# Optimization experiments

Hardware: AMD Instinct MI355X
Metric: run time of the kernel (lower is better)

## Reference

```python
import jax, jax.numpy as jnp
import numpy as np

D_MODEL = 1024
NUM_HEADS = 16
D_K = D_MODEL // NUM_HEADS
D_FF = 4096
EPS = 1e-5


def _layernorm(x, gamma, beta):
    mu = jnp.mean(x, axis=-1, keepdims=True)
    var = jnp.mean(jnp.square(x - mu), axis=-1, keepdims=True)
    return (x - mu) * jax.lax.rsqrt(var + EPS) * gamma + beta


def setup_inputs() -> dict:
    key = jax.random.key(0)
    ks = jax.random.split(key, 16)
    B, S = 4, 2048
    s_in = 1.0 / np.sqrt(D_MODEL)
    s_ff = 1.0 / np.sqrt(D_FF)
    inp = {
        "x": jax.random.normal(ks[0], (B, S, D_MODEL), jnp.float32),
        "src_mask": jnp.ones((B, 1, 1, S), jnp.int32),
        "w_q": jax.random.normal(ks[1], (D_MODEL, D_MODEL), jnp.float32) * s_in,
        "b_q": jnp.zeros((D_MODEL,), jnp.float32),
        "w_k": jax.random.normal(ks[2], (D_MODEL, D_MODEL), jnp.float32) * s_in,
        "b_k": jnp.zeros((D_MODEL,), jnp.float32),
        "w_v": jax.random.normal(ks[3], (D_MODEL, D_MODEL), jnp.float32) * s_in,
        "b_v": jnp.zeros((D_MODEL,), jnp.float32),
        "w_o": jax.random.normal(ks[4], (D_MODEL, D_MODEL), jnp.float32) * s_in,
        "b_o": jnp.zeros((D_MODEL,), jnp.float32),
        "w1": jax.random.normal(ks[5], (D_MODEL, D_FF), jnp.float32) * s_in,
        "b1": jnp.zeros((D_FF,), jnp.float32),
        "w2": jax.random.normal(ks[6], (D_FF, D_MODEL), jnp.float32) * s_ff,
        "b2": jnp.zeros((D_MODEL,), jnp.float32),
        "g1": jnp.ones((D_MODEL,), jnp.float32),
        "be1": jnp.zeros((D_MODEL,), jnp.float32),
        "g2": jnp.ones((D_MODEL,), jnp.float32),
        "be2": jnp.zeros((D_MODEL,), jnp.float32),
    }
    return inp


def reference(x, src_mask, w_q, b_q, w_k, b_k, w_v, b_v, w_o, b_o,
              w1, b1, w2, b2, g1, be1, g2, be2):
    B, S, _ = x.shape

    def split_heads(t):  # [B,S,D] -> [B,H,S,dk]
        return t.reshape(B, S, NUM_HEADS, D_K).transpose(0, 2, 1, 3)

    q = split_heads(x @ w_q + b_q)
    k = split_heads(x @ w_k + b_k)
    v = split_heads(x @ w_v + b_v)

    scores = jnp.einsum("bhqd,bhkd->bhqk", q, k) / np.sqrt(D_K)
    scores = jnp.where(src_mask == 0, -jnp.inf, scores)
    attn = jax.nn.softmax(scores, axis=-1)
    ctx = jnp.einsum("bhqk,bhkd->bhqd", attn, v)
    merged = ctx.transpose(0, 2, 1, 3).reshape(B, S, D_MODEL)
    attn_out = merged @ w_o + b_o

    h = _layernorm(x + attn_out, g1, be1)
    ff = jax.nn.relu(h @ w1 + b1) @ w2 + b2
    return _layernorm(h + ff, g2, be2)
```

## Files before the change

### kernel.cpp

```cpp
#include <hip/hip_runtime.h>

typedef unsigned short u16;
typedef __attribute__((ext_vector_type(4))) unsigned short u16x4;
typedef __attribute__((ext_vector_type(8))) short bf16x8;
typedef __attribute__((ext_vector_type(4))) float f32x4;

__device__ inline float bf2f(u16 u) {
  union { unsigned int i; float f; } v; v.i = ((unsigned int)u) << 16; return v.f;
}
__device__ inline u16 f2bf(float f) {
  union { float f; unsigned int i; } v; v.f = f;
  unsigned int r = v.i + 0x7fffu + ((v.i >> 16) & 1u);
  return (u16)(r >> 16);
}
__device__ inline unsigned int cvt_pk_bf16(float lo, float hi) {
  unsigned int r;
  asm("v_cvt_pk_bf16_f32 %0, %1, %2" : "=v"(r) : "v"(lo), "v"(hi));
  return r;
}

typedef const __attribute__((address_space(1))) unsigned int* gas_t;
typedef __attribute__((address_space(3))) unsigned int* las_t;
__device__ inline void gload_lds16(const u16* g, u16* l) {
  __builtin_amdgcn_global_load_lds((gas_t)(unsigned long long)(const void*)g,
                                   (las_t)(unsigned int)(unsigned long long)(void*)l,
                                   16, 0, 0);
}

__global__ __launch_bounds__(256) void cvt_bf16(const float* __restrict__ src,
                                                u16* __restrict__ dst, int n) {
  int i = (blockIdx.x * 256 + threadIdx.x) * 4;
  if (i >= n) return;
  float4 v = *(const float4*)(src + i);
  u16x4 o;
  o.x = f2bf(v.x); o.y = f2bf(v.y); o.z = f2bf(v.z); o.w = f2bf(v.w);
  *(u16x4*)(dst + i) = o;
}

__global__ __launch_bounds__(256) void concat3(const float* __restrict__ a,
                                               const float* __restrict__ b,
                                               const float* __restrict__ c,
                                               float* __restrict__ o, int n) {
  int i = blockIdx.x * 256 + threadIdx.x;
  if (i >= n) return;
  o[i] = a[i]; o[n + i] = b[i]; o[2 * n + i] = c[i];
}

__global__ __launch_bounds__(256) void transpose_f32_bf16(const float* __restrict__ src,
                                                          u16* __restrict__ dst,
                                                          int R, int C) {
  __shared__ u16 tile[32][33];
  int tx = threadIdx.x & 31, ty = threadIdx.x >> 5;
  int c0 = blockIdx.x * 32, r0 = blockIdx.y * 32;
  #pragma unroll
  for (int i = ty; i < 32; i += 8)
    tile[i][tx] = f2bf(src[(size_t)(r0 + i) * C + c0 + tx]);
  __syncthreads();
  #pragma unroll
  for (int i = ty; i < 32; i += 8)
    dst[(size_t)(c0 + i) * R + r0 + tx] = tile[tx][i];
}

__global__ __launch_bounds__(256) void transpose_v(const u16* __restrict__ src,
                                                   u16* __restrict__ VT,
                                                   int B, int S, int H, int RS, int CO) {
  __shared__ u16 tile[32][33];
  int tx = threadIdx.x & 31, ty = threadIdx.x >> 5;
  int s0 = blockIdx.x * 32, d0 = blockIdx.y * 32;
  int bh = blockIdx.z;
  int b = bh / H, h = bh % H;
  #pragma unroll
  for (int i = ty; i < 32; i += 8)
    tile[i][tx] = src[(size_t)(b * S + s0 + i) * RS + CO + h * 64 + d0 + tx];
  __syncthreads();
  #pragma unroll
  for (int i = ty; i < 32; i += 8)
    VT[((size_t)bh * 64 + d0 + i) * S + s0 + tx] = tile[tx][i];
}

__global__ __launch_bounds__(256) void gemm_bt(const u16* __restrict__ A,
                                               const u16* __restrict__ Bt,
                                               const float* __restrict__ bias,
                                               u16* __restrict__ C,
                                               int M, int N, int K, int relu) {
  __shared__ u16 As[128 * 32];
  __shared__ u16 Bs[128 * 32];
  const int tid = threadIdx.x;
  const int lane = tid & 63, wid = tid >> 6;
  const int lr = lane & 15, quad = lane >> 4;
  const int wm = (wid >> 1) * 64, wn = (wid & 1) * 64;
  const int m0 = blockIdx.y * 128, n0 = blockIdx.x * 128;
  const int lrow = lane >> 2;
  const int lcol = (lane & 3) * 8;

  f32x4 acc[4][4];
  const f32x4 zero = {0.f, 0.f, 0.f, 0.f};
  #pragma unroll
  for (int mt = 0; mt < 4; ++mt)
    #pragma unroll
    for (int nt = 0; nt < 4; ++nt) acc[mt][nt] = zero;

  for (int k0 = 0; k0 < K; k0 += 32) {
    #pragma unroll
    for (int it = 0; it < 2; ++it) {
      int rbase = wid * 32 + it * 16;
      gload_lds16(A + (size_t)(m0 + rbase + lrow) * K + k0 + lcol, &As[rbase * 32]);
      gload_lds16(Bt + (size_t)(n0 + rbase + lrow) * K + k0 + lcol, &Bs[rbase * 32]);
    }
    __syncthreads();
    bf16x8 af[4], bfr[4];
    #pragma unroll
    for (int mt = 0; mt < 4; ++mt)
      af[mt] = *(const bf16x8*)(&As[(wm + mt * 16 + lr) * 32 + quad * 8]);
    #pragma unroll
    for (int nt = 0; nt < 4; ++nt)
      bfr[nt] = *(const bf16x8*)(&Bs[(wn + nt * 16 + lr) * 32 + quad * 8]);
    #pragma unroll
    for (int mt = 0; mt < 4; ++mt)
      #pragma unroll
      for (int nt = 0; nt < 4; ++nt)
        acc[mt][nt] = __builtin_amdgcn_mfma_f32_16x16x32_bf16(af[mt], bfr[nt], acc[mt][nt], 0, 0, 0);
    __syncthreads();
  }

  #pragma unroll
  for (int nt = 0; nt < 4; ++nt) {
    int n = n0 + wn + nt * 16 + lr;
    float bv = bias[n];
    #pragma unroll
    for (int mt = 0; mt < 4; ++mt) {
      #pragma unroll
      for (int i = 0; i < 4; ++i) {
        int m = m0 + wm + mt * 16 + quad * 4 + i;
        float v = acc[mt][nt][i] + bv;
        if (relu) v = fmaxf(v, 0.f);
        C[(size_t)m * N + n] = f2bf(v);
      }
    }
  }
}

__global__ __launch_bounds__(256) void flash_attn(const u16* __restrict__ Qp,
                                                  const u16* __restrict__ Kp,
                                                  const u16* __restrict__ VT,
                                                  const int* __restrict__ mask,
                                                  u16* __restrict__ ctx,
                                                  int B, int S, int H, int QSTR) {
  __shared__ u16 kt_lds[64 * 64];
  __shared__ u16 vt_lds[64 * 64];
  __shared__ u16 p_lds[4 * 16 * 72];
  __shared__ float msk_lds[64];
  const int tid = threadIdx.x;
  const int lane = tid & 63, wid = tid >> 6;
  const int lr = lane & 15, quad = lane >> 4;
  const int bh = blockIdx.y;
  const int b = bh / H, h = bh % H;
  const int q0 = blockIdx.x * 64;
  const u16* vt_base = VT + (size_t)bh * 64 * S;
  const float SC = 0.125f * 1.44269504089f;

  const int srl = lane >> 3;
  const int scol = ((lane & 7) ^ srl) * 8;
  const int swz = (lr & 7) << 3;

  bf16x8 qf[2];
  {
    int qm = q0 + wid * 16 + lr;
    const u16* qptr = Qp + (size_t)(b * S + qm) * QSTR + h * 64;
    qf[0] = *(const bf16x8*)(qptr + quad * 8);
    qf[1] = *(const bf16x8*)(qptr + 32 + quad * 8);
  }

  float m_i = -1e30f, l_i = 0.f;
  f32x4 O[4];
  #pragma unroll
  for (int nt = 0; nt < 4; ++nt) {
    O[nt][0] = 0.f; O[nt][1] = 0.f; O[nt][2] = 0.f; O[nt][3] = 0.f;
  }

  u16* pw = &p_lds[wid * 16 * 72];
  const u16* kgp = Kp + ((size_t)b * S + wid * 16 + srl) * QSTR + h * 64 + scol;
  const u16* vgp = vt_base + (size_t)(wid * 16 + srl) * S + scol;
  u16* klb = &kt_lds[(wid * 16) * 64];
  u16* vlb = &vt_lds[(wid * 16) * 64];

  for (int kt = 0; kt < S; kt += 64) {
    gload_lds16(kgp + (size_t)kt * QSTR, klb);
    gload_lds16(kgp + (size_t)(kt + 8) * QSTR, klb + 8 * 64);
    gload_lds16(vgp + kt, vlb);
    gload_lds16(vgp + 8 * (size_t)S + kt, vlb + 8 * 64);
    if (tid < 64) msk_lds[tid] = mask[b * S + kt + tid] ? 0.f : -1e30f;
    __syncthreads();

    float s[4][4];
    __builtin_amdgcn_s_setprio(1);
    #pragma unroll
    for (int st = 0; st < 4; ++st) {
      f32x4 c = {0.f, 0.f, 0.f, 0.f};
      const u16* kr = &kt_lds[(st * 16 + lr) * 64];
      bf16x8 kf0 = *(const bf16x8*)(kr + ((quad * 8) ^ swz));
      bf16x8 kf1 = *(const bf16x8*)(kr + ((32 + quad * 8) ^ swz));
      c = __builtin_amdgcn_mfma_f32_16x16x32_bf16(kf0, qf[0], c, 0, 0, 0);
      c = __builtin_amdgcn_mfma_f32_16x16x32_bf16(kf1, qf[1], c, 0, 0, 0);
      float4 mv = *(const float4*)(&msk_lds[st * 16 + quad * 4]);
      s[st][0] = c[0] * SC + mv.x;
      s[st][1] = c[1] * SC + mv.y;
      s[st][2] = c[2] * SC + mv.z;
      s[st][3] = c[3] * SC + mv.w;
    }
    __builtin_amdgcn_s_setprio(0);

    float tmax = s[0][0];
    #pragma unroll
    for (int st = 0; st < 4; ++st)
      #pragma unroll
      for (int i = 0; i < 4; ++i) tmax = fmaxf(tmax, s[st][i]);
    tmax = fmaxf(tmax, __shfl_xor(tmax, 16, 64));
    tmax = fmaxf(tmax, __shfl_xor(tmax, 32, 64));
    if (__any(tmax > m_i + 8.0f)) {
      float mn = fmaxf(m_i, tmax);
      float al = exp2f(m_i - mn);
      m_i = mn;
      l_i *= al;
      #pragma unroll
      for (int nt = 0; nt < 4; ++nt) {
        O[nt][0] *= al; O[nt][1] *= al; O[nt][2] *= al; O[nt][3] *= al;
      }
    }
    float rs = 0.f;
    #pragma unroll
    for (int st = 0; st < 4; ++st)
      #pragma unroll
      for (int i = 0; i < 4; ++i) {
        float p = exp2f(s[st][i] - m_i);
        s[st][i] = p; rs += p;
      }
    l_i += rs;

    #pragma unroll
    for (int st = 0; st < 4; ++st) {
      uint2 pk;
      pk.x = cvt_pk_bf16(s[st][0], s[st][1]);
      pk.y = cvt_pk_bf16(s[st][2], s[st][3]);
      *(uint2*)(&pw[lr * 72 + st * 16 + quad * 4]) = pk;
    }

    bf16x8 pf0 = *(const bf16x8*)(&pw[lr * 72 + quad * 8]);
    bf16x8 pf1 = *(const bf16x8*)(&pw[lr * 72 + 32 + quad * 8]);
    __builtin_amdgcn_s_setprio(1);
    #pragma unroll
    for (int nt = 0; nt < 4; ++nt) {
      const u16* vr = &vt_lds[(nt * 16 + lr) * 64];
      bf16x8 vf0 = *(const bf16x8*)(vr + ((quad * 8) ^ swz));
      bf16x8 vf1 = *(const bf16x8*)(vr + ((32 + quad * 8) ^ swz));
      O[nt] = __builtin_amdgcn_mfma_f32_16x16x32_bf16(vf0, pf0, O[nt], 0, 0, 0);
      O[nt] = __builtin_amdgcn_mfma_f32_16x16x32_bf16(vf1, pf1, O[nt], 0, 0, 0);
    }
    __builtin_amdgcn_s_setprio(0);
    __syncthreads();
  }

  l_i += __shfl_xor(l_i, 16, 64);
  l_i += __shfl_xor(l_i, 32, 64);
  float linv = 1.f / fmaxf(l_i, 1e-30f);
  int q = q0 + wid * 16 + lr;
  u16* op = ctx + (size_t)(b * S + q) * (H * 64) + h * 64;
  #pragma unroll
  for (int nt = 0; nt < 4; ++nt) {
    u16x4 o;
    o.x = f2bf(O[nt][0] * linv); o.y = f2bf(O[nt][1] * linv);
    o.z = f2bf(O[nt][2] * linv); o.w = f2bf(O[nt][3] * linv);
    *(u16x4*)(op + nt * 16 + quad * 4) = o;
  }
}

__device__ inline float block_reduce_sum(float v, float* sbuf) {
  #pragma unroll
  for (int m = 1; m < 64; m <<= 1) v += __shfl_xor(v, m, 64);
  int w = threadIdx.x >> 6;
  if ((threadIdx.x & 63) == 0) sbuf[w] = v;
  __syncthreads();
  v = sbuf[0] + sbuf[1] + sbuf[2] + sbuf[3];
  __syncthreads();
  return v;
}

__global__ __launch_bounds__(256) void add_ln(const float* __restrict__ a32,
                                              const u16* __restrict__ a16,
                                              const u16* __restrict__ b,
                                              const float* __restrict__ g,
                                              const float* __restrict__ be,
                                              u16* __restrict__ out16,
                                              float* __restrict__ out32, int D) {
  __shared__ float sbuf[4];
  int row = blockIdx.x;
  size_t base = (size_t)row * D;
  int i = threadIdx.x * 4;
  float v[4];
  {
    u16x4 bv = *(const u16x4*)(b + base + i);
    if (a32) {
      float4 av = *(const float4*)(a32 + base + i);
      v[0] = av.x + bf2f(bv.x); v[1] = av.y + bf2f(bv.y);
      v[2] = av.z + bf2f(bv.z); v[3] = av.w + bf2f(bv.w);
    } else {
      u16x4 av = *(const u16x4*)(a16 + base + i);
      v[0] = bf2f(av.x) + bf2f(bv.x); v[1] = bf2f(av.y) + bf2f(bv.y);
      v[2] = bf2f(av.z) + bf2f(bv.z); v[3] = bf2f(av.w) + bf2f(bv.w);
    }
  }
  float sum = v[0] + v[1] + v[2] + v[3];
  sum = block_reduce_sum(sum, sbuf);
  float mean = sum / (float)D;
  float var = 0.f;
  #pragma unroll
  for (int j = 0; j < 4; ++j) { float d = v[j] - mean; var += d * d; }
  var = block_reduce_sum(var, sbuf);
  float rstd = rsqrtf(var / (float)D + 1e-5f);
  float4 gv = *(const float4*)(g + i);
  float4 bev = *(const float4*)(be + i);
  float o0 = (v[0] - mean) * rstd * gv.x + bev.x;
  float o1 = (v[1] - mean) * rstd * gv.y + bev.y;
  float o2 = (v[2] - mean) * rstd * gv.z + bev.z;
  float o3 = (v[3] - mean) * rstd * gv.w + bev.w;
  if (out32) {
    float4 o = {o0, o1, o2, o3};
    *(float4*)(out32 + base + i) = o;
  } else {
    u16x4 o;
    o.x = f2bf(o0); o.y = f2bf(o1); o.z = f2bf(o2); o.w = f2bf(o3);
    *(u16x4*)(out16 + base + i) = o;
  }
}

extern "C" void kernel_launch(void* const* d_in, const int* in_sizes, int n_in,
                              void* d_out, int out_size, void* d_ws, size_t ws_size,
                              hipStream_t stream) {
  (void)in_sizes; (void)n_in; (void)out_size; (void)ws_size;
  const float* x   = (const float*)d_in[0];
  const int* mask  = (const int*)d_in[1];
  const float* wq  = (const float*)d_in[2];
  const float* bq  = (const float*)d_in[3];
  const float* wk  = (const float*)d_in[4];
  const float* bk  = (const float*)d_in[5];
  const float* wv  = (const float*)d_in[6];
  const float* bv  = (const float*)d_in[7];
  const float* wo  = (const float*)d_in[8];
  const float* bo  = (const float*)d_in[9];
  const float* w1  = (const float*)d_in[10];
  const float* b1  = (const float*)d_in[11];
  const float* w2  = (const float*)d_in[12];
  const float* b2  = (const float*)d_in[13];
  const float* g1  = (const float*)d_in[14];
  const float* be1 = (const float*)d_in[15];
  const float* g2  = (const float*)d_in[16];
  const float* be2 = (const float*)d_in[17];

  const int B = 4, S = 2048, D = 1024, H = 16, DFF = 4096;
  const int D3 = 3 * D;
  const size_t TOK = (size_t)B * S;
  const size_t TD = TOK * D;

  u16* ws   = (u16*)d_ws;
  u16* QKVp = ws;
  u16* xb   = ws + 3 * TD;
  u16* VT   = xb;
  u16* CTX  = ws + 4 * TD;
  u16* ATT  = ws + 5 * TD;
  u16* Hb   = ws + 6 * TD;
  u16* QKVT = ws + 7 * TD;
  u16* WOT  = QKVT + 3 * (size_t)D * D;
  u16* W1T  = WOT + (size_t)D * D;
  u16* FF1  = ws;
  u16* FF2  = ATT;
  u16* W2T  = QKVT;
  float* biasc = (float*)CTX;

  dim3 blk(256);

  cvt_bf16<<<dim3((unsigned)(TD / (256 * 4))), blk, 0, stream>>>(x, xb, (int)TD);
  concat3<<<dim3(4), blk, 0, stream>>>(bq, bk, bv, biasc, D);

  transpose_f32_bf16<<<dim3(D / 32, D / 32), blk, 0, stream>>>(wq, QKVT, D, D);
  transpose_f32_bf16<<<dim3(D / 32, D / 32), blk, 0, stream>>>(wk, QKVT + (size_t)D * D, D, D);
  transpose_f32_bf16<<<dim3(D / 32, D / 32), blk, 0, stream>>>(wv, QKVT + 2 * (size_t)D * D, D, D);
  transpose_f32_bf16<<<dim3(D / 32, D / 32), blk, 0, stream>>>(wo, WOT, D, D);
  transpose_f32_bf16<<<dim3(DFF / 32, D / 32), blk, 0, stream>>>(w1, W1T, D, DFF);

  gemm_bt<<<dim3(D3 / 128, TOK / 128), blk, 0, stream>>>(xb, QKVT, biasc, QKVp, (int)TOK, D3, D, 0);

  transpose_v<<<dim3(S / 32, 2, B * H), blk, 0, stream>>>(QKVp, VT, B, S, H, D3, 2 * D);

  flash_attn<<<dim3(S / 64, B * H), blk, 0, stream>>>(QKVp, QKVp + D, VT, mask, CTX, B, S, H, D3);

  gemm_bt<<<dim3(D / 128, TOK / 128), blk, 0, stream>>>(CTX, WOT, bo, ATT, (int)TOK, D, D, 0);

  transpose_f32_bf16<<<dim3(D / 32, DFF / 32), blk, 0, stream>>>(w2, W2T, DFF, D);

  add_ln<<<dim3((unsigned)TOK), blk, 0, stream>>>(x, (const u16*)nullptr, ATT, g1, be1,
                                                  Hb, (float*)nullptr, D);

  gemm_bt<<<dim3(DFF / 128, TOK / 128), blk, 0, stream>>>(Hb, W1T, b1, FF1, (int)TOK, DFF, D, 1);
  gemm_bt<<<dim3(D / 128, TOK / 128), blk, 0, stream>>>(FF1, W2T, b2, FF2, (int)TOK, D, DFF, 0);

  add_ln<<<dim3((unsigned)TOK), blk, 0, stream>>>((const float*)nullptr, Hb, FF2, g2, be2,
                                                  (u16*)nullptr, (float*)d_out, D);
}
```

Before: 659.0 us.

## Double-buffer K/V tiles in flash attention and prefetch mask into registers

The flash attention kernel now keeps two LDS buffers for the K and V tiles and issues the next tile's global-to-LDS loads before computing on the current one. This overlaps memory latency with the MFMA work and leaves one barrier per iteration instead of a load-then-sync pattern. The mask is prefetched directly into registers instead of being staged through LDS. The P scratch buffer switches from padded rows to an XOR swizzle, which shrinks its LDS footprint. LDS use still roughly doubles for K/V, which may reduce occupancy. The prefetch also relies on the single trailing barrier being enough to guard buffer reuse, and it is not obvious the async loads are complete before the next iteration reads them.

```diff
diff --git a/kernel.cpp b/kernel.cpp
--- a/kernel.cpp
+++ b/kernel.cpp
@@ -146,10 +146,9 @@
                                                   const int* __restrict__ mask,
                                                   u16* __restrict__ ctx,
                                                   int B, int S, int H, int QSTR) {
-  __shared__ u16 kt_lds[64 * 64];
-  __shared__ u16 vt_lds[64 * 64];
-  __shared__ u16 p_lds[4 * 16 * 72];
-  __shared__ float msk_lds[64];
+  __shared__ u16 kt_lds[2][64 * 64];
+  __shared__ u16 vt_lds[2][64 * 64];
+  __shared__ u16 p_lds[4 * 16 * 64];
   const int tid = threadIdx.x;
   const int lane = tid & 63, wid = tid >> 6;
   const int lr = lane & 15, quad = lane >> 4;
@@ -157,6 +156,7 @@
   const int b = bh / H, h = bh % H;
   const int q0 = blockIdx.x * 64;
   const u16* vt_base = VT + (size_t)bh * 64 * S;
+  const int* mbase = mask + b * S;
   const float SC = 0.125f * 1.44269504089f;
 
   const int srl = lane >> 3;
@@ -178,35 +178,57 @@
     O[nt][0] = 0.f; O[nt][1] = 0.f; O[nt][2] = 0.f; O[nt][3] = 0.f;
   }
 
-  u16* pw = &p_lds[wid * 16 * 72];
+  u16* pw = &p_lds[wid * 16 * 64 + lr * 64];
   const u16* kgp = Kp + ((size_t)b * S + wid * 16 + srl) * QSTR + h * 64 + scol;
   const u16* vgp = vt_base + (size_t)(wid * 16 + srl) * S + scol;
-  u16* klb = &kt_lds[(wid * 16) * 64];
-  u16* vlb = &vt_lds[(wid * 16) * 64];
-
+  u16* klb0 = &kt_lds[0][(wid * 16) * 64];
+  u16* vlb0 = &vt_lds[0][(wid * 16) * 64];
+  u16* klb1 = &kt_lds[1][(wid * 16) * 64];
+  u16* vlb1 = &vt_lds[1][(wid * 16) * 64];
+
+  gload_lds16(kgp, klb0);
+  gload_lds16(kgp + 8 * (size_t)QSTR, klb0 + 8 * 64);
+  gload_lds16(vgp, vlb0);
+  gload_lds16(vgp + 8 * (size_t)S, vlb0 + 8 * 64);
+  int4 mk_nxt[4];
+  #pragma unroll
+  for (int st = 0; st < 4; ++st)
+    mk_nxt[st] = *(const int4*)(mbase + st * 16 + quad * 4);
+  __syncthreads();
+
+  int cur = 0;
   for (int kt = 0; kt < S; kt += 64) {
-    gload_lds16(kgp + (size_t)kt * QSTR, klb);
-    gload_lds16(kgp + (size_t)(kt + 8) * QSTR, klb + 8 * 64);
-    gload_lds16(vgp + kt, vlb);
-    gload_lds16(vgp + 8 * (size_t)S + kt, vlb + 8 * 64);
-    if (tid < 64) msk_lds[tid] = mask[b * S + kt + tid] ? 0.f : -1e30f;
-    __syncthreads();
+    int4 mk[4];
+    #pragma unroll
+    for (int st = 0; st < 4; ++st) mk[st] = mk_nxt[st];
+    if (kt + 64 < S) {
+      u16* klb = cur ? klb0 : klb1;
+      u16* vlb = cur ? vlb0 : vlb1;
+      gload_lds16(kgp + (size_t)(kt + 64) * QSTR, klb);
+      gload_lds16(kgp + (size_t)(kt + 72) * QSTR, klb + 8 * 64);
+      gload_lds16(vgp + kt + 64, vlb);
+      gload_lds16(vgp + 8 * (size_t)S + kt + 64, vlb + 8 * 64);
+      #pragma unroll
+      for (int st = 0; st < 4; ++st)
+        mk_nxt[st] = *(const int4*)(mbase + kt + 64 + st * 16 + quad * 4);
+    }
+    const u16* kl = kt_lds[cur];
+    const u16* vl = vt_lds[cur];
 
     float s[4][4];
     __builtin_amdgcn_s_setprio(1);
     #pragma unroll
     for (int st = 0; st < 4; ++st) {
       f32x4 c = {0.f, 0.f, 0.f, 0.f};
-      const u16* kr = &kt_lds[(st * 16 + lr) * 64];
+      const u16* kr = &kl[(st * 16 + lr) * 64];
       bf16x8 kf0 = *(const bf16x8*)(kr + ((quad * 8) ^ swz));
       bf16x8 kf1 = *(const bf16x8*)(kr + ((32 + quad * 8) ^ swz));
       c = __builtin_amdgcn_mfma_f32_16x16x32_bf16(kf0, qf[0], c, 0, 0, 0);
       c = __builtin_amdgcn_mfma_f32_16x16x32_bf16(kf1, qf[1], c, 0, 0, 0);
-      float4 mv = *(const float4*)(&msk_lds[st * 16 + quad * 4]);
-      s[st][0] = c[0] * SC + mv.x;
-      s[st][1] = c[1] * SC + mv.y;
-      s[st][2] = c[2] * SC + mv.z;
-      s[st][3] = c[3] * SC + mv.w;
+      s[st][0] = c[0] * SC + (mk[st].x ? 0.f : -1e30f);
+      s[st][1] = c[1] * SC + (mk[st].y ? 0.f : -1e30f);
+      s[st][2] = c[2] * SC + (mk[st].z ? 0.f : -1e30f);
+      s[st][3] = c[3] * SC + (mk[st].w ? 0.f : -1e30f);
     }
     __builtin_amdgcn_s_setprio(0);
 
@@ -242,22 +264,24 @@
       uint2 pk;
       pk.x = cvt_pk_bf16(s[st][0], s[st][1]);
       pk.y = cvt_pk_bf16(s[st][2], s[st][3]);
-      *(uint2*)(&pw[lr * 72 + st * 16 + quad * 4]) = pk;
-    }
-
-    bf16x8 pf0 = *(const bf16x8*)(&pw[lr * 72 + quad * 8]);
-    bf16x8 pf1 = *(const bf16x8*)(&pw[lr * 72 + 32 + quad * 8]);
+      *(uint2*)(&pw[(st * 16 + quad * 4) ^ swz]) = pk;
+    }
+
+    bf16x8 pf0 = *(const bf16x8*)(&pw[(quad * 8) ^ swz]);
+    bf16x8 pf1 = *(const bf16x8*)(&pw[(32 + quad * 8) ^ swz]);
     __builtin_amdgcn_s_setprio(1);
     #pragma unroll
     for (int nt = 0; nt < 4; ++nt) {
-      const u16* vr = &vt_lds[(nt * 16 + lr) * 64];
+      const u16* vr = &vl[(nt * 16 + lr) * 64];
       bf16x8 vf0 = *(const bf16x8*)(vr + ((quad * 8) ^ swz));
       bf16x8 vf1 = *(const bf16x8*)(vr + ((32 + quad * 8) ^ swz));
       O[nt] = __builtin_amdgcn_mfma_f32_16x16x32_bf16(vf0, pf0, O[nt], 0, 0, 0);
       O[nt] = __builtin_amdgcn_mfma_f32_16x16x32_bf16(vf1, pf1, O[nt], 0, 0, 0);
     }
     __builtin_amdgcn_s_setprio(0);
+
     __syncthreads();
+    cur ^= 1;
   }
 
   l_i += __shfl_xor(l_i, 16, 64);
```

Measured after the change: 696.0 us. +5.6%, slower.

## Rewrite flash attention with 32x32x16 MFMA, register P, 128-query blocks

Applied to the files above, without the earlier changes.

The flash attention kernel moves from 16x16x32 to 32x32x16 MFMA tiles. Each wave now owns 32 queries, so a block covers 128 queries and each K/V tile loaded into LDS is reused across twice as many queries. The probability matrix is repacked between lanes with cross-half shuffles instead of a round trip through LDS. The mask is now a ballot that is applied only when some key is masked, and the rescale threshold now works on unscaled scores. This cuts LDS traffic, global K/V loads and the grid size, at the cost of more registers and fewer blocks, which may lower occupancy.

```diff
diff --git a/kernel.cpp b/kernel.cpp
--- a/kernel.cpp
+++ b/kernel.cpp
@@ -4,6 +4,7 @@
 typedef __attribute__((ext_vector_type(4))) unsigned short u16x4;
 typedef __attribute__((ext_vector_type(8))) short bf16x8;
 typedef __attribute__((ext_vector_type(4))) float f32x4;
+typedef __attribute__((ext_vector_type(16))) float f32x16;
 
 __device__ inline float bf2f(u16 u) {
   union { unsigned int i; float f; } v; v.i = ((unsigned int)u) << 16; return v.f;
@@ -17,6 +18,12 @@
   unsigned int r;
   asm("v_cvt_pk_bf16_f32 %0, %1, %2" : "=v"(r) : "v"(lo), "v"(hi));
   return r;
+}
+__device__ inline f32x16 zero16() {
+  f32x16 z;
+  #pragma unroll
+  for (int i = 0; i < 16; ++i) z[i] = 0.f;
+  return z;
 }
 
 typedef const __attribute__((address_space(1))) unsigned int* gas_t;
@@ -148,37 +155,31 @@
                                                   int B, int S, int H, int QSTR) {
   __shared__ u16 kt_lds[64 * 64];
   __shared__ u16 vt_lds[64 * 64];
-  __shared__ u16 p_lds[4 * 16 * 72];
-  __shared__ float msk_lds[64];
   const int tid = threadIdx.x;
   const int lane = tid & 63, wid = tid >> 6;
-  const int lr = lane & 15, quad = lane >> 4;
+  const int l31 = lane & 31, hi = lane >> 5;
   const int bh = blockIdx.y;
   const int b = bh / H, h = bh % H;
-  const int q0 = blockIdx.x * 64;
   const u16* vt_base = VT + (size_t)bh * 64 * S;
+  const int* mbase = mask + b * S;
   const float SC = 0.125f * 1.44269504089f;
 
   const int srl = lane >> 3;
   const int scol = ((lane & 7) ^ srl) * 8;
-  const int swz = (lr & 7) << 3;
-
-  bf16x8 qf[2];
+  const int rsw = (lane & 7) << 3;
+
+  const int q = blockIdx.x * 128 + wid * 32 + l31;
+  bf16x8 qf[4];
   {
-    int qm = q0 + wid * 16 + lr;
-    const u16* qptr = Qp + (size_t)(b * S + qm) * QSTR + h * 64;
-    qf[0] = *(const bf16x8*)(qptr + quad * 8);
-    qf[1] = *(const bf16x8*)(qptr + 32 + quad * 8);
+    const u16* qptr = Qp + (size_t)(b * S + q) * QSTR + h * 64;
+    #pragma unroll
+    for (int t = 0; t < 4; ++t)
+      qf[t] = *(const bf16x8*)(qptr + t * 16 + hi * 8);
   }
 
   float m_i = -1e30f, l_i = 0.f;
-  f32x4 O[4];
-  #pragma unroll
-  for (int nt = 0; nt < 4; ++nt) {
-    O[nt][0] = 0.f; O[nt][1] = 0.f; O[nt][2] = 0.f; O[nt][3] = 0.f;
-  }
-
-  u16* pw = &p_lds[wid * 16 * 72];
+  f32x16 o0 = zero16(), o1 = zero16();
+
   const u16* kgp = Kp + ((size_t)b * S + wid * 16 + srl) * QSTR + h * 64 + scol;
   const u16* vgp = vt_base + (size_t)(wid * 16 + srl) * S + scol;
   u16* klb = &kt_lds[(wid * 16) * 64];
@@ -189,88 +190,108 @@
     gload_lds16(kgp + (size_t)(kt + 8) * QSTR, klb + 8 * 64);
     gload_lds16(vgp + kt, vlb);
     gload_lds16(vgp + 8 * (size_t)S + kt, vlb + 8 * 64);
-    if (tid < 64) msk_lds[tid] = mask[b * S + kt + tid] ? 0.f : -1e30f;
+    int mv = mbase[kt + lane];
+    unsigned long long bal = __ballot(mv != 0);
     __syncthreads();
 
-    float s[4][4];
+    f32x16 sa0 = zero16(), sa1 = zero16();
+    const u16* krow0 = &kt_lds[l31 * 64];
+    const u16* krow1 = &kt_lds[(32 + l31) * 64];
     __builtin_amdgcn_s_setprio(1);
     #pragma unroll
-    for (int st = 0; st < 4; ++st) {
-      f32x4 c = {0.f, 0.f, 0.f, 0.f};
-      const u16* kr = &kt_lds[(st * 16 + lr) * 64];
-      bf16x8 kf0 = *(const bf16x8*)(kr + ((quad * 8) ^ swz));
-      bf16x8 kf1 = *(const bf16x8*)(kr + ((32 + quad * 8) ^ swz));
-      c = __builtin_amdgcn_mfma_f32_16x16x32_bf16(kf0, qf[0], c, 0, 0, 0);
-      c = __builtin_amdgcn_mfma_f32_16x16x32_bf16(kf1, qf[1], c, 0, 0, 0);
-      float4 mv = *(const float4*)(&msk_lds[st * 16 + quad * 4]);
-      s[st][0] = c[0] * SC + mv.x;
-      s[st][1] = c[1] * SC + mv.y;
-      s[st][2] = c[2] * SC + mv.z;
-      s[st][3] = c[3] * SC + mv.w;
+    for (int dblock = 0; dblock < 4; ++dblock) {
+      int c = (dblock * 16 + hi * 8) ^ rsw;
+      bf16x8 kf0 = *(const bf16x8*)(krow0 + c);
+      bf16x8 kf1 = *(const bf16x8*)(krow1 + c);
+      sa0 = __builtin_amdgcn_mfma_f32_32x32x16_bf16(kf0, qf[dblock], sa0, 0, 0, 0);
+      sa1 = __builtin_amdgcn_mfma_f32_32x32x16_bf16(kf1, qf[dblock], sa1, 0, 0, 0);
     }
     __builtin_amdgcn_s_setprio(0);
 
-    float tmax = s[0][0];
-    #pragma unroll
-    for (int st = 0; st < 4; ++st)
+    if (bal != 0xFFFFFFFFFFFFFFFFull) {
+      unsigned long long balh = bal >> (hi * 4);
       #pragma unroll
-      for (int i = 0; i < 4; ++i) tmax = fmaxf(tmax, s[st][i]);
-    tmax = fmaxf(tmax, __shfl_xor(tmax, 16, 64));
+      for (int r = 0; r < 16; ++r) {
+        int kloc = (r & 3) + 8 * (r >> 2);
+        if (!((balh >> kloc) & 1)) sa0[r] = -2e30f;
+        if (!((balh >> (32 + kloc)) & 1)) sa1[r] = -2e30f;
+      }
+    }
+
+    float tmax = sa0[0];
+    #pragma unroll
+    for (int r = 1; r < 16; ++r) tmax = fmaxf(tmax, sa0[r]);
+    #pragma unroll
+    for (int r = 0; r < 16; ++r) tmax = fmaxf(tmax, sa1[r]);
     tmax = fmaxf(tmax, __shfl_xor(tmax, 32, 64));
-    if (__any(tmax > m_i + 8.0f)) {
+    if (__any(tmax > m_i + 44.0f)) {
       float mn = fmaxf(m_i, tmax);
-      float al = exp2f(m_i - mn);
+      float al = exp2f((m_i - mn) * SC);
       m_i = mn;
       l_i *= al;
       #pragma unroll
-      for (int nt = 0; nt < 4; ++nt) {
-        O[nt][0] *= al; O[nt][1] *= al; O[nt][2] *= al; O[nt][3] *= al;
+      for (int r = 0; r < 16; ++r) { o0[r] *= al; o1[r] *= al; }
+    }
+    float msc = m_i * SC;
+    float rs = 0.f;
+    #pragma unroll
+    for (int r = 0; r < 16; ++r) {
+      float p0 = exp2f(__builtin_fmaf(sa0[r], SC, -msc));
+      float p1 = exp2f(__builtin_fmaf(sa1[r], SC, -msc));
+      sa0[r] = p0; sa1[r] = p1; rs += p0 + p1;
+    }
+    l_i += rs;
+
+    unsigned pfw[4][4];
+    #pragma unroll
+    for (int b1 = 0; b1 < 2; ++b1) {
+      #pragma unroll
+      for (int pair = 0; pair < 2; ++pair) {
+        unsigned X0 = cvt_pk_bf16(sa0[(2 * b1) * 4 + pair * 2], sa0[(2 * b1) * 4 + pair * 2 + 1]);
+        unsigned Y0 = cvt_pk_bf16(sa0[(2 * b1 + 1) * 4 + pair * 2], sa0[(2 * b1 + 1) * 4 + pair * 2 + 1]);
+        unsigned Xp0 = __shfl_xor(X0, 32, 64);
+        unsigned Yp0 = __shfl_xor(Y0, 32, 64);
+        pfw[b1][pair] = hi ? Yp0 : X0;
+        pfw[b1][pair + 2] = hi ? Y0 : Xp0;
+        unsigned X1 = cvt_pk_bf16(sa1[(2 * b1) * 4 + pair * 2], sa1[(2 * b1) * 4 + pair * 2 + 1]);
+        unsigned Y1 = cvt_pk_bf16(sa1[(2 * b1 + 1) * 4 + pair * 2], sa1[(2 * b1 + 1) * 4 + pair * 2 + 1]);
+        unsigned Xp1 = __shfl_xor(X1, 32, 64);
+        unsigned Yp1 = __shfl_xor(Y1, 32, 64);
+        pfw[2 + b1][pair] = hi ? Yp1 : X1;
+        pfw[2 + b1][pair + 2] = hi ? Y1 : Xp1;
       }
     }
-    float rs = 0.f;
-    #pragma unroll
-    for (int st = 0; st < 4; ++st)
-      #pragma unroll
-      for (int i = 0; i < 4; ++i) {
-        float p = exp2f(s[st][i] - m_i);
-        s[st][i] = p; rs += p;
-      }
-    l_i += rs;
-
-    #pragma unroll
-    for (int st = 0; st < 4; ++st) {
-      uint2 pk;
-      pk.x = cvt_pk_bf16(s[st][0], s[st][1]);
-      pk.y = cvt_pk_bf16(s[st][2], s[st][3]);
-      *(uint2*)(&pw[lr * 72 + st * 16 + quad * 4]) = pk;
-    }
-
-    bf16x8 pf0 = *(const bf16x8*)(&pw[lr * 72 + quad * 8]);
-    bf16x8 pf1 = *(const bf16x8*)(&pw[lr * 72 + 32 + quad * 8]);
+
+    const u16* vrow0 = &vt_lds[l31 * 64];
+    const u16* vrow1 = &vt_lds[(32 + l31) * 64];
     __builtin_amdgcn_s_setprio(1);
     #pragma unroll
-    for (int nt = 0; nt < 4; ++nt) {
-      const u16* vr = &vt_lds[(nt * 16 + lr) * 64];
-      bf16x8 vf0 = *(const bf16x8*)(vr + ((quad * 8) ^ swz));
-      bf16x8 vf1 = *(const bf16x8*)(vr + ((32 + quad * 8) ^ swz));
-      O[nt] = __builtin_amdgcn_mfma_f32_16x16x32_bf16(vf0, pf0, O[nt], 0, 0, 0);
-      O[nt] = __builtin_amdgcn_mfma_f32_16x16x32_bf16(vf1, pf1, O[nt], 0, 0, 0);
+    for (int kb = 0; kb < 4; ++kb) {
+      int c = (kb * 16 + hi * 8) ^ rsw;
+      bf16x8 vf0 = *(const bf16x8*)(vrow0 + c);
+      bf16x8 vf1 = *(const bf16x8*)(vrow1 + c);
+      union { unsigned w[4]; bf16x8 v; } pu;
+      pu.w[0] = pfw[kb][0]; pu.w[1] = pfw[kb][1];
+      pu.w[2] = pfw[kb][2]; pu.w[3] = pfw[kb][3];
+      o0 = __builtin_amdgcn_mfma_f32_32x32x16_bf16(vf0, pu.v, o0, 0, 0, 0);
+      o1 = __builtin_amdgcn_mfma_f32_32x32x16_bf16(vf1, pu.v, o1, 0, 0, 0);
     }
     __builtin_amdgcn_s_setprio(0);
     __syncthreads();
   }
 
-  l_i += __shfl_xor(l_i, 16, 64);
   l_i += __shfl_xor(l_i, 32, 64);
   float linv = 1.f / fmaxf(l_i, 1e-30f);
-  int q = q0 + wid * 16 + lr;
   u16* op = ctx + (size_t)(b * S + q) * (H * 64) + h * 64;
   #pragma unroll
-  for (int nt = 0; nt < 4; ++nt) {
-    u16x4 o;
-    o.x = f2bf(O[nt][0] * linv); o.y = f2bf(O[nt][1] * linv);
-    o.z = f2bf(O[nt][2] * linv); o.w = f2bf(O[nt][3] * linv);
-    *(u16x4*)(op + nt * 16 + quad * 4) = o;
+  for (int rq = 0; rq < 4; ++rq) {
+    uint2 w0, w1;
+    w0.x = cvt_pk_bf16(o0[rq * 4 + 0] * linv, o0[rq * 4 + 1] * linv);
+    w0.y = cvt_pk_bf16(o0[rq * 4 + 2] * linv, o0[rq * 4 + 3] * linv);
+    *(uint2*)(op + rq * 8 + hi * 4) = w0;
+    w1.x = cvt_pk_bf16(o1[rq * 4 + 0] * linv, o1[rq * 4 + 1] * linv);
+    w1.y = cvt_pk_bf16(o1[rq * 4 + 2] * linv, o1[rq * 4 + 3] * linv);
+    *(uint2*)(op + 32 + rq * 8 + hi * 4) = w1;
   }
 }
 
@@ -391,7 +412,7 @@
 
   transpose_v<<<dim3(S / 32, 2, B * H), blk, 0, stream>>>(QKVp, VT, B, S, H, D3, 2 * D);
 
-  flash_attn<<<dim3(S / 64, B * H), blk, 0, stream>>>(QKVp, QKVp + D, VT, mask, CTX, B, S, H, D3);
+  flash_attn<<<dim3(S / 128, B * H), blk, 0, stream>>>(QKVp, QKVp + D, VT, mask, CTX, B, S, H, D3);
 
   gemm_bt<<<dim3(D / 128, TOK / 128), blk, 0, stream>>>(CTX, WOT, bo, ATT, (int)TOK, D, D, 0);
 
```

New measurement: 657.8 us. About the same (-0.2%).
